# Kernel optimization log

Measured on AMD Instinct MI355X. Metric: run time of the kernel, lower is better.

## Reference

```python
import jax, jax.numpy as jnp
import numpy as np

EPS = 1e-12  # torch F.normalize eps


def _normalize(x):
    n = jnp.sqrt(jnp.sum(x * x, axis=1, keepdims=True))
    return x / jnp.maximum(n, EPS)


def _exp_sim(a, b, temp):
    # exp(a @ b.T / temp); returns (diag [B], row_sum [B,1])
    m = jnp.exp(jnp.matmul(a, b.T) / temp)
    return jnp.diagonal(m), jnp.sum(m, axis=1, keepdims=True)


def reference(x):
    temp = 0.1
    bsz = x.shape[0] // 3
    xn = _normalize(x)
    xe, ye, ze = xn[:bsz], xn[bsz:2 * bsz], xn[2 * bsz:]

    d_xx, s_xx = _exp_sim(xe, xe, temp)
    d_yy, s_yy = _exp_sim(ye, ye, temp)
    d_xy, s_xy = _exp_sim(xe, ye, temp)
    d_ax, s_ax = _exp_sim(xe, ze, temp)
    d_ay, s_ay = _exp_sim(ye, ze, temp)
    d_zx, s_zx = _exp_sim(ze, xe, temp)
    d_zy, s_zy = _exp_sim(ze, ye, temp)

    # NOTE: diag terms are [B], row-sums are [B,1] -> denominator broadcasts to
    # [B,B], matching the original torch broadcasting exactly.
    denom_mutual = (s_xy - d_xy) + (s_xx - d_xx) + (s_yy - d_yy)  # [B,B]
    loss_mutual = jnp.mean(-2.0 * jnp.log(d_xy / denom_mutual))

    def aux(d, s):
        return jnp.mean(-jnp.log(d / (s - d)))  # d/[B,B] -> [B,B]

    loss = (loss_mutual + aux(d_ax, s_ax) + aux(d_ay, s_ay)
            + aux(d_zx, s_zx) + aux(d_zy, s_zy))
    return loss


def setup_inputs() -> dict:
    key = jax.random.key(0)
    x = jax.random.normal(key, (12288, 128), dtype=jnp.float32)
    return {"x": x}
```

## Files before the change

kernel.cpp:

```cpp
#include <hip/hip_runtime.h>
#include <hip/hip_bf16.h>


typedef __attribute__((ext_vector_type(8))) short short8;
typedef __attribute__((ext_vector_type(4))) float floatx4;

#define D   128
#define BSZ 4096
#define GPM 256
#define GRID_EXPSIM (5 * 32 * 8)

__global__ __launch_bounds__(256) void normalize_kernel(
    const float* __restrict__ x, __hip_bfloat162* __restrict__ xnf2,
    float* __restrict__ out, int rows) {
  int tid = threadIdx.x;
  if (blockIdx.x == 0 && tid == 0) out[0] = 0.0f;

  int row  = blockIdx.x * 4 + (tid >> 6);
  int lane = tid & 63;
  if (row >= rows) return;
  const float2* xr = (const float2*)(x + (size_t)row * D);
  float2 v = xr[lane];
  float s = v.x * v.x + v.y * v.y;
#pragma unroll
  for (int off = 1; off < 64; off <<= 1) s += __shfl_xor(s, off, 64);
  float scale = 3.7982825470322528f / fmaxf(sqrtf(s), 1e-12f);
  __hip_bfloat162 h;
  h.x = __float2bfloat16(v.x * scale);
  h.y = __float2bfloat16(v.y * scale);
  int g    = row >> 4;
  int kk   = lane >> 4;
  int quad = (lane >> 2) & 3;
  int jj   = lane & 3;
  xnf2[g * 1024 + kk * 256 + (quad * 16 + (row & 15)) * 4 + jj] = h;
}

template <bool COL, bool DIAG>
__device__ __forceinline__ void epilogue(
    const floatx4 (&acc)[2][4], float (&rs)[2][4], float (&cs)[4],
    int rowg0, int colg0, int quad, int lm, float* __restrict__ diag_ptr) {
#pragma unroll
  for (int mi = 0; mi < 2; mi++) {
#pragma unroll
    for (int r = 0; r < 4; r++) {
      int rowg = rowg0 + mi * 16 + quad * 4 + r;
      float part = 0.f;
#pragma unroll
      for (int ni = 0; ni < 4; ni++) {
        float e = __builtin_amdgcn_exp2f(acc[mi][ni][r]);
        part += e;
        if (COL) cs[ni] += e;
        if (DIAG) {
          if (colg0 + ni * 16 + lm == rowg) diag_ptr[rowg] = e;
        }
      }
      rs[mi][r] += part;
    }
  }
}

__global__ __launch_bounds__(256) void expsim_kernel(
    const short8* __restrict__ xnf8,
    float* __restrict__ srow,
    float* __restrict__ scol,
    float* __restrict__ diag) {
  __shared__ float csLDS[4 * 512];

  int tid = threadIdx.x;
  int bx  = blockIdx.x;
  int task = bx >> 8;
  int rem  = bx & 255;
  int ib   = rem >> 3;
  int jsp  = rem & 7;

  const int aoff_t[5] = {0, 1, 0, 0, 1};
  const int boff_t[5] = {0, 1, 1, 2, 2};
  bool col_en = (task >= 3);

  int w    = tid >> 6;
  int lane = tid & 63;
  int quad = lane >> 4;
  int lm   = lane & 15;
  int rowg0 = ib * 128 + w * 32;

  bool dgblk = (jsp == (ib >> 2));
  int  tdiag = ((ib & 3) * 2) + (w >> 1);

  float* diag_ptr = diag + task * BSZ;

  int gA = aoff_t[task] * GPM + ib * 8 + w * 2;
  short8 afrag[2][4];
#pragma unroll
  for (int mi = 0; mi < 2; mi++)
#pragma unroll
    for (int kk = 0; kk < 4; kk++)
      afrag[mi][kk] = xnf8[(size_t)(gA + mi) * 256 + kk * 64 + lane];

  float rs[2][4];
#pragma unroll
  for (int mi = 0; mi < 2; mi++)
#pragma unroll
    for (int r = 0; r < 4; r++) rs[mi][r] = 0.0f;

  const floatx4 z4 = {0.f, 0.f, 0.f, 0.f};
  const short8* bbase = xnf8 + (size_t)(boff_t[task] * GPM + jsp * 32) * 256 + lane;

  short8 bf[16];
#pragma unroll
  for (int i = 0; i < 16; i++)
    bf[i] = bbase[(size_t)(i & 3) * 256 + (i >> 2) * 64];

#pragma unroll 1
  for (int t = 0; t < 8; t++) {
    int colg0 = (jsp * 8 + t) * 64;
    floatx4 acc[2][4];
#pragma unroll
    for (int kk = 0; kk < 4; kk++) {
#pragma unroll
      for (int mi = 0; mi < 2; mi++)
#pragma unroll
        for (int ni = 0; ni < 4; ni++)
          acc[mi][ni] = __builtin_amdgcn_mfma_f32_16x16x32_bf16(
              afrag[mi][kk], bf[kk * 4 + ni], (kk == 0) ? z4 : acc[mi][ni],
              0, 0, 0);
      if (t < 7) {
#pragma unroll
        for (int ni = 0; ni < 4; ni++)
          bf[kk * 4 + ni] = bbase[(size_t)((t + 1) * 4 + ni) * 256 + kk * 64];
      }
    }

    float cs[4] = {0.f, 0.f, 0.f, 0.f};
    bool dg = dgblk && (t == tdiag);
    if (col_en) {
      if (dg) epilogue<true, true>(acc, rs, cs, rowg0, colg0, quad, lm, diag_ptr);
      else    epilogue<true, false>(acc, rs, cs, rowg0, colg0, quad, lm, diag_ptr);
#pragma unroll
      for (int ni = 0; ni < 4; ni++) {
        float v = cs[ni];
        v += __shfl_xor(v, 16, 64);
        v += __shfl_xor(v, 32, 64);
        if (quad == 0) csLDS[w * 512 + t * 64 + ni * 16 + lm] = v;
      }
    } else {
      if (dg) epilogue<false, true>(acc, rs, cs, rowg0, colg0, quad, lm, diag_ptr);
      else    epilogue<false, false>(acc, rs, cs, rowg0, colg0, quad, lm, diag_ptr);
    }
  }

  float* srow_ptr = srow + ((size_t)(task * 8 + jsp)) * BSZ;
#pragma unroll
  for (int mi = 0; mi < 2; mi++) {
#pragma unroll
    for (int r = 0; r < 4; r++) {
      float v = rs[mi][r];
      v += __shfl_xor(v, 1, 64);
      v += __shfl_xor(v, 2, 64);
      v += __shfl_xor(v, 4, 64);
      v += __shfl_xor(v, 8, 64);
      if (lm == 0) srow_ptr[rowg0 + mi * 16 + quad * 4 + r] = v;
    }
  }

  if (col_en) {
    __syncthreads();
    float* scol_ptr = scol + ((size_t)((task - 3) * 32 + ib)) * BSZ + jsp * 512;
    for (int c = tid; c < 512; c += 256)
      scol_ptr[c] = csLDS[c] + csLDS[512 + c] + csLDS[1024 + c] + csLDS[1536 + c];
  }
}

__global__ __launch_bounds__(256) void reduce_kernel(
    const float* __restrict__ srow, const float* __restrict__ scol,
    const float* __restrict__ diag, float* __restrict__ out) {
  int tid = threadIdx.x;
  int i   = blockIdx.x * 256 + tid;

  float s[5];
#pragma unroll
  for (int t = 0; t < 5; t++) {
    float a = 0.f;
#pragma unroll
    for (int js = 0; js < 8; js++) a += srow[(size_t)(t * 8 + js) * BSZ + i];
    s[t] = a;
  }
  float s_zx = 0.f, s_zy = 0.f;
#pragma unroll 8
  for (int ib = 0; ib < 32; ib++) {
    s_zx += scol[(size_t)ib * BSZ + i];
    s_zy += scol[(size_t)(32 + ib) * BSZ + i];
  }
  float d_xx = diag[0 * BSZ + i], d_yy = diag[1 * BSZ + i];
  float d_xy = diag[2 * BSZ + i], d_ax = diag[3 * BSZ + i];
  float d_ay = diag[4 * BSZ + i];

  float denom = (s[2] - d_xy) + (s[0] - d_xx) + (s[1] - d_yy);
  float tloc = -2.0f * __logf(d_xy / denom);
  tloc -= __logf(d_ax / (s[3] - d_ax));
  tloc -= __logf(d_ay / (s[4] - d_ay));
  tloc -= __logf(d_ax / (s_zx - d_ax));
  tloc -= __logf(d_ay / (s_zy - d_ay));

  __shared__ float red[256];
  red[tid] = tloc;
  __syncthreads();
  for (int st = 128; st > 0; st >>= 1) {
    if (tid < st) red[tid] += red[tid + st];
    __syncthreads();
  }
  if (tid == 0) atomicAdd(out, red[0] / (float)BSZ);
}

extern "C" void kernel_launch(void* const* d_in, const int* in_sizes, int n_in,
                              void* d_out, int out_size, void* d_ws, size_t ws_size,
                              hipStream_t stream) {
  const float* x = (const float*)d_in[0];
  int rows = in_sizes[0] / D;

  char*  ws       = (char*)d_ws;
  short* xnf      = (short*)ws;
  size_t xn_bytes = (size_t)rows * D * sizeof(short);
  float* srow     = (float*)(ws + xn_bytes);
  float* scol     = srow + 5 * 8 * BSZ;
  float* diag     = scol + 2 * 32 * BSZ;

  normalize_kernel<<<rows / 4, 256, 0, stream>>>(
      x, (__hip_bfloat162*)xnf, (float*)d_out, rows);
  expsim_kernel<<<GRID_EXPSIM, 256, 0, stream>>>(
      (const short8*)xnf, srow, scol, diag);
  reduce_kernel<<<16, 256, 0, stream>>>(srow, scol, diag, (float*)d_out);
}
```

Before: 99.29 us.

## Retile expsim to 256x256 blocks with 64-row warp tiles

Changes the block tile from 128 rows by 512 columns to 256 by 256, giving each warp 64 rows (4x4 MFMA tiles) so every B fragment load feeds twice as many MFMAs. The software prefetch of the next B tile during the MFMA loop is dropped; B is now loaded at the start of each column step. Partial row and column sum buffers and the reduce kernel are resized to match. Register pressure roughly doubles for accumulators and A fragments, which may lower occupancy, and load latency is no longer overlapped with compute.

```diff
diff --git a/kernel.cpp b/kernel.cpp
--- a/kernel.cpp
+++ b/kernel.cpp
@@ -8,7 +8,7 @@
 #define D   128
 #define BSZ 4096
 #define GPM 256
-#define GRID_EXPSIM (5 * 32 * 8)
+#define GRID_EXPSIM (5 * 16 * 16)
 
 __global__ __launch_bounds__(256) void normalize_kernel(
     const float* __restrict__ x, __hip_bfloat162* __restrict__ xnf2,
@@ -37,10 +37,10 @@
 
 template <bool COL, bool DIAG>
 __device__ __forceinline__ void epilogue(
-    const floatx4 (&acc)[2][4], float (&rs)[2][4], float (&cs)[4],
+    const floatx4 (&acc)[4][4], float (&rs)[4][4], float (&cs)[4],
     int rowg0, int colg0, int quad, int lm, float* __restrict__ diag_ptr) {
 #pragma unroll
-  for (int mi = 0; mi < 2; mi++) {
+  for (int mi = 0; mi < 4; mi++) {
 #pragma unroll
     for (int r = 0; r < 4; r++) {
       int rowg = rowg0 + mi * 16 + quad * 4 + r;
@@ -64,14 +64,14 @@
     float* __restrict__ srow,
     float* __restrict__ scol,
     float* __restrict__ diag) {
-  __shared__ float csLDS[4 * 512];
+  __shared__ float csLDS[4 * 256];
 
   int tid = threadIdx.x;
   int bx  = blockIdx.x;
   int task = bx >> 8;
   int rem  = bx & 255;
-  int ib   = rem >> 3;
-  int jsp  = rem & 7;
+  int rb   = rem >> 4;
+  int cb   = rem & 15;
 
   const int aoff_t[5] = {0, 1, 0, 0, 1};
   const int boff_t[5] = {0, 1, 1, 2, 2};
@@ -81,57 +81,51 @@
   int lane = tid & 63;
   int quad = lane >> 4;
   int lm   = lane & 15;
-  int rowg0 = ib * 128 + w * 32;
-
-  bool dgblk = (jsp == (ib >> 2));
-  int  tdiag = ((ib & 3) * 2) + (w >> 1);
+  int rowg0 = rb * 256 + w * 64;
+
+  bool dgblk = (rb == cb);
 
   float* diag_ptr = diag + task * BSZ;
 
-  int gA = aoff_t[task] * GPM + ib * 8 + w * 2;
-  short8 afrag[2][4];
-#pragma unroll
-  for (int mi = 0; mi < 2; mi++)
+  int gA = aoff_t[task] * GPM + rb * 16 + w * 4;
+  short8 afrag[4][4];
+#pragma unroll
+  for (int mi = 0; mi < 4; mi++)
 #pragma unroll
     for (int kk = 0; kk < 4; kk++)
       afrag[mi][kk] = xnf8[(size_t)(gA + mi) * 256 + kk * 64 + lane];
 
-  float rs[2][4];
-#pragma unroll
-  for (int mi = 0; mi < 2; mi++)
+  float rs[4][4];
+#pragma unroll
+  for (int mi = 0; mi < 4; mi++)
 #pragma unroll
     for (int r = 0; r < 4; r++) rs[mi][r] = 0.0f;
 
   const floatx4 z4 = {0.f, 0.f, 0.f, 0.f};
-  const short8* bbase = xnf8 + (size_t)(boff_t[task] * GPM + jsp * 32) * 256 + lane;
-
-  short8 bf[16];
-#pragma unroll
-  for (int i = 0; i < 16; i++)
-    bf[i] = bbase[(size_t)(i & 3) * 256 + (i >> 2) * 64];
+  const short8* bbase = xnf8 + (size_t)(boff_t[task] * GPM + cb * 16) * 256 + lane;
 
 #pragma unroll 1
-  for (int t = 0; t < 8; t++) {
-    int colg0 = (jsp * 8 + t) * 64;
-    floatx4 acc[2][4];
-#pragma unroll
-    for (int kk = 0; kk < 4; kk++) {
-#pragma unroll
-      for (int mi = 0; mi < 2; mi++)
+  for (int t = 0; t < 4; t++) {
+    int colg0 = cb * 256 + t * 64;
+
+    short8 bf[16];
+#pragma unroll
+    for (int i = 0; i < 16; i++)
+      bf[i] = bbase[(size_t)(t * 4 + (i & 3)) * 256 + (i >> 2) * 64];
+
+    floatx4 acc[4][4];
+#pragma unroll
+    for (int kk = 0; kk < 4; kk++)
+#pragma unroll
+      for (int mi = 0; mi < 4; mi++)
 #pragma unroll
         for (int ni = 0; ni < 4; ni++)
           acc[mi][ni] = __builtin_amdgcn_mfma_f32_16x16x32_bf16(
               afrag[mi][kk], bf[kk * 4 + ni], (kk == 0) ? z4 : acc[mi][ni],
               0, 0, 0);
-      if (t < 7) {
-#pragma unroll
-        for (int ni = 0; ni < 4; ni++)
-          bf[kk * 4 + ni] = bbase[(size_t)((t + 1) * 4 + ni) * 256 + kk * 64];
-      }
-    }
 
     float cs[4] = {0.f, 0.f, 0.f, 0.f};
-    bool dg = dgblk && (t == tdiag);
+    bool dg = dgblk && (t == w);
     if (col_en) {
       if (dg) epilogue<true, true>(acc, rs, cs, rowg0, colg0, quad, lm, diag_ptr);
       else    epilogue<true, false>(acc, rs, cs, rowg0, colg0, quad, lm, diag_ptr);
@@ -140,7 +134,7 @@
         float v = cs[ni];
         v += __shfl_xor(v, 16, 64);
         v += __shfl_xor(v, 32, 64);
-        if (quad == 0) csLDS[w * 512 + t * 64 + ni * 16 + lm] = v;
+        if (quad == 0) csLDS[w * 256 + t * 64 + ni * 16 + lm] = v;
       }
     } else {
       if (dg) epilogue<false, true>(acc, rs, cs, rowg0, colg0, quad, lm, diag_ptr);
@@ -148,9 +142,9 @@
     }
   }
 
-  float* srow_ptr = srow + ((size_t)(task * 8 + jsp)) * BSZ;
-#pragma unroll
-  for (int mi = 0; mi < 2; mi++) {
+  float* srow_ptr = srow + ((size_t)(task * 16 + cb)) * BSZ;
+#pragma unroll
+  for (int mi = 0; mi < 4; mi++) {
 #pragma unroll
     for (int r = 0; r < 4; r++) {
       float v = rs[mi][r];
@@ -164,9 +158,8 @@
 
   if (col_en) {
     __syncthreads();
-    float* scol_ptr = scol + ((size_t)((task - 3) * 32 + ib)) * BSZ + jsp * 512;
-    for (int c = tid; c < 512; c += 256)
-      scol_ptr[c] = csLDS[c] + csLDS[512 + c] + csLDS[1024 + c] + csLDS[1536 + c];
+    float* scol_ptr = scol + ((size_t)((task - 3) * 16 + rb)) * BSZ + cb * 256;
+    scol_ptr[tid] = csLDS[tid] + csLDS[256 + tid] + csLDS[512 + tid] + csLDS[768 + tid];
   }
 }
 
@@ -181,14 +174,14 @@
   for (int t = 0; t < 5; t++) {
     float a = 0.f;
 #pragma unroll
-    for (int js = 0; js < 8; js++) a += srow[(size_t)(t * 8 + js) * BSZ + i];
+    for (int js = 0; js < 16; js++) a += srow[(size_t)(t * 16 + js) * BSZ + i];
     s[t] = a;
   }
   float s_zx = 0.f, s_zy = 0.f;
 #pragma unroll 8
-  for (int ib = 0; ib < 32; ib++) {
+  for (int ib = 0; ib < 16; ib++) {
     s_zx += scol[(size_t)ib * BSZ + i];
-    s_zy += scol[(size_t)(32 + ib) * BSZ + i];
+    s_zy += scol[(size_t)(16 + ib) * BSZ + i];
   }
   float d_xx = diag[0 * BSZ + i], d_yy = diag[1 * BSZ + i];
   float d_xy = diag[2 * BSZ + i], d_ax = diag[3 * BSZ + i];
@@ -221,8 +214,8 @@
   short* xnf      = (short*)ws;
   size_t xn_bytes = (size_t)rows * D * sizeof(short);
   float* srow     = (float*)(ws + xn_bytes);
-  float* scol     = srow + 5 * 8 * BSZ;
-  float* diag     = scol + 2 * 32 * BSZ;
+  float* scol     = srow + 5 * 16 * BSZ;
+  float* diag     = scol + 2 * 16 * BSZ;
 
   normalize_kernel<<<rows / 4, 256, 0, stream>>>(
       x, (__hip_bfloat162*)xnf, (float*)d_out, rows);
```

After: 97.21 us. -2.1%, faster.
